# Optimization experiments

Hardware: AMD Instinct MI355X
Metric: run time of the kernel (lower is better)

## Reference

```python
import jax, jax.numpy as jnp
import numpy as np

B, N, DQ, DK, DV, H = 8, 1024, 512, 512, 512, 8
DH = DV // H  # 64


def setup_inputs() -> dict:
    key = jax.random.key(0)
    ks = jax.random.split(key, 12)
    Q = jax.random.normal(ks[0], (B, N, DQ), jnp.float32)
    K = jax.random.normal(ks[1], (B, N, DK), jnp.float32)
    U = jax.random.normal(ks[2], (H, N, N, B), jnp.float32) * 0.1  # additive bias, [H,Nq,Nk,B]
    mask = (jax.random.uniform(ks[3], (B, N)) < 0.9).astype(jnp.float32)
    w = 0.02
    return {
        'Q': Q, 'K': K, 'U': U, 'mask': mask,
        'Wq': jax.random.normal(ks[4], (DQ, DV), jnp.float32) * w,
        'bq': jnp.zeros((DV,), jnp.float32),
        'Wk': jax.random.normal(ks[5], (DK, DV), jnp.float32) * w,
        'bk': jnp.zeros((DV,), jnp.float32),
        'Wv': jax.random.normal(ks[6], (DK, DV), jnp.float32) * w,
        'bv': jnp.zeros((DV,), jnp.float32),
        'Wo': jax.random.normal(ks[7], (DV, DV), jnp.float32) * w,
        'bo': jnp.zeros((DV,), jnp.float32),
    }


def reference(Q, K, U, mask, Wq, bq, Wk, bk, Wv, bv, Wo, bo):
    m = mask[:, :, None]  # [B,N,1]
    q = (Q @ Wq + bq) * m  # [B,N,DV]
    k = (K @ Wk + bk) * m
    v = (K @ Wv + bv) * m
    # split heads: torch.cat(split(dh,2),0) is head-major -> [H,B,N,DH]
    qh = q.reshape(B, N, H, DH).transpose(2, 0, 1, 3)
    kh = k.reshape(B, N, H, DH).transpose(2, 0, 1, 3)
    vh = v.reshape(B, N, H, DH).transpose(2, 0, 1, 3)
    # U.transpose(1,3).transpose(-1,-2).reshape(H*B,N,N) == transpose(U,(0,3,1,2))
    bias = jnp.transpose(U, (0, 3, 1, 2))  # [H,B,Nq,Nk]
    scores = jnp.einsum('hbid,hbjd->hbij', qh, kh) / np.sqrt(DV) + bias
    # custom double-masked softmax (max taken over unmasked scores, faithfully)
    max_elem = jnp.max(scores, axis=3, keepdims=True)
    m1 = mask[None, :, :, None]  # [1,B,Nq,1]
    m2 = mask[None, :, None, :]  # [1,B,1,Nk]
    num = jnp.exp((scores - max_elem) * m1 * m2) * m1 * m2
    A = num / (jnp.sum(num, axis=3, keepdims=True) + 1e-16)
    o = qh + jnp.einsum('hbij,hbjd->hbid', A, vh)  # residual, [H,B,N,DH]
    O = o.transpose(1, 2, 0, 3).reshape(B, N, DV)  # merge heads
    O = O + jax.nn.relu((O @ Wo + bo) * m)
    return O
```

## Files before the change

### kernel.cpp

```cpp
#include <hip/hip_runtime.h>

#define B_   8
#define N_   1024
#define D_   512
#define H_   8
#define DH_  64
#define SCALE_ 0.044194173824159216f
#define LOG2E_ 1.4426950408889634f

typedef __attribute__((ext_vector_type(8))) short bf16x8;
typedef __attribute__((ext_vector_type(4))) float f32x4;
typedef __attribute__((ext_vector_type(8))) unsigned short us8;
typedef __attribute__((ext_vector_type(4))) unsigned int u32x4;

__device__ __forceinline__ unsigned short f2bf(float f) {
  unsigned u = __builtin_bit_cast(unsigned, f);
  u += 0x7fffu + ((u >> 16) & 1u);
  return (unsigned short)(u >> 16);
}
__device__ __forceinline__ float bf2f(unsigned short h) {
  unsigned u = ((unsigned)h) << 16;
  return __builtin_bit_cast(float, u);
}
__device__ __forceinline__ void gl_lds16(const void* g, void* l) {
  __builtin_amdgcn_global_load_lds(
      (const __attribute__((address_space(1))) unsigned int*)g,
      (__attribute__((address_space(3))) unsigned int*)l, 16, 0, 0);
}
__device__ __forceinline__ unsigned cvt_pk_bf16(float lo, float hi) {
  unsigned r;
  asm("v_cvt_pk_bf16_f32 %0, %1, %2" : "=v"(r) : "v"(lo), "v"(hi));
  return r;
}
#define MFMA16(a, b, c) __builtin_amdgcn_mfma_f32_16x16x32_bf16((a), (b), (c), 0, 0, 0)

__global__ void prep_w(const float* __restrict__ Wq, const float* __restrict__ Wk,
                       const float* __restrict__ Wv, const float* __restrict__ Wo,
                       unsigned short* __restrict__ WT) {
  int idx = blockIdx.x * 256 + threadIdx.x;
  int mat = idx >> 18;
  int rem = idx & 0x3FFFF;
  int k = rem >> 9, n = rem & 511;
  const float* W = (mat == 0) ? Wq : (mat == 1) ? Wk : (mat == 2) ? Wv : Wo;
  float v = W[(size_t)k * 512 + n];
  int kmap = (k & ~63) | ((k & 63) ^ ((n & 7) << 3));
  WT[(size_t)mat * 262144 + (size_t)n * 512 + kmap] = f2bf(v);
}

#define GEMM_BODY(A, W, bias, EPILOGUE)                                          \
  __shared__ unsigned short Alds[2][128][72];                                    \
  __shared__ unsigned short Blds[2][128 * 64];                                   \
  const int t = threadIdx.x, w = t >> 6, l = t & 63;                             \
  const int wr = w >> 1, wc = w & 1;                                             \
  const int lm = l & 15, lg = l >> 4;                                            \
  const int bm = blockIdx.x >> 2, bn = blockIdx.x & 3;                           \
  f32x4 acc[4][4];                                                               \
  _Pragma("unroll") for (int mt = 0; mt < 4; ++mt)                               \
  _Pragma("unroll") for (int nt = 0; nt < 4; ++nt)                               \
      acc[mt][nt] = f32x4{0.f, 0.f, 0.f, 0.f};                                   \
  float4 areg[8];                                                                \
  auto loadA = [&](int kt) {                                                     \
    _Pragma("unroll") for (int p = 0; p < 8; ++p) {                              \
      int row = (t >> 4) + p * 16, col = (t & 15) * 4;                           \
      areg[p] = *(const float4*)&A[((size_t)(bm * 128 + row)) * 512 + kt * 64 + col]; \
    }                                                                            \
  };                                                                             \
  auto issueB = [&](int kt, int sb) {                                            \
    _Pragma("unroll") for (int p = 0; p < 4; ++p) {                              \
      int chunk = w * 4 + p;                                                     \
      int row = chunk * 8 + (l >> 3), gc = kt * 64 + (l & 7) * 8;                \
      gl_lds16(&W[((size_t)(bn * 128 + row)) * 512 + gc],                        \
               &Blds[sb][chunk * 512 + l * 8]);                                  \
    }                                                                            \
  };                                                                             \
  auto writeA = [&](int sb) {                                                    \
    _Pragma("unroll") for (int p = 0; p < 8; ++p) {                              \
      int row = (t >> 4) + p * 16, col = (t & 15) * 4;                           \
      float4 v = areg[p];                                                        \
      uint2 d;                                                                   \
      d.x = (unsigned)f2bf(v.x) | ((unsigned)f2bf(v.y) << 16);                   \
      d.y = (unsigned)f2bf(v.z) | ((unsigned)f2bf(v.w) << 16);                   \
      *(uint2*)&Alds[sb][row][col] = d;                                          \
    }                                                                            \
  };                                                                             \
  loadA(0); issueB(0, 0); writeA(0);                                             \
  __syncthreads();                                                               \
  int buf = 0;                                                                   \
  for (int kt = 0; kt < 8; ++kt) {                                               \
    if (kt + 1 < 8) { loadA(kt + 1); issueB(kt + 1, buf ^ 1); }                  \
    _Pragma("unroll") for (int kk = 0; kk < 2; ++kk) {                           \
      bf16x8 af[4], bfv[4];                                                      \
      _Pragma("unroll") for (int mt = 0; mt < 4; ++mt)                           \
        af[mt] = *(const bf16x8*)&Alds[buf][wr * 64 + mt * 16 + lm][kk * 32 + lg * 8]; \
      _Pragma("unroll") for (int nt = 0; nt < 4; ++nt) {                         \
        int rr = wc * 64 + nt * 16 + lm;                                         \
        int c = (kk * 32 + lg * 8) ^ ((rr & 7) << 3);                            \
        bfv[nt] = *(const bf16x8*)&Blds[buf][rr * 64 + c];                       \
      }                                                                          \
      _Pragma("unroll") for (int mt = 0; mt < 4; ++mt)                           \
      _Pragma("unroll") for (int nt = 0; nt < 4; ++nt)                           \
          acc[mt][nt] = MFMA16(af[mt], bfv[nt], acc[mt][nt]);                    \
    }                                                                            \
    if (kt + 1 < 8) writeA(buf ^ 1);                                             \
    __syncthreads();                                                             \
    buf ^= 1;                                                                    \
  }                                                                              \
  _Pragma("unroll") for (int mt = 0; mt < 4; ++mt)                               \
  _Pragma("unroll") for (int nt = 0; nt < 4; ++nt) {                             \
    int gn = bn * 128 + wc * 64 + nt * 16 + lm;                                  \
    float bv_ = bias[gn];                                                        \
    _Pragma("unroll") for (int e = 0; e < 4; ++e) {                              \
      int gm = bm * 128 + wr * 64 + mt * 16 + lg * 4 + e;                        \
      float v = acc[mt][nt][e] + bv_;                                            \
      size_t off = (size_t)gm * 512 + gn;                                        \
      EPILOGUE                                                                   \
    }                                                                            \
  }

__global__ __launch_bounds__(256, 2) void gemm_proj3(
    const float* __restrict__ Q, const float* __restrict__ K,
    const unsigned short* __restrict__ WT,
    const float* __restrict__ bq, const float* __restrict__ bk,
    const float* __restrict__ bv, const float* __restrict__ mask,
    unsigned short* __restrict__ qb, unsigned short* __restrict__ kb,
    unsigned short* __restrict__ vtmp) {
  const int mat = blockIdx.y;
  const float* A = (mat == 0) ? Q : K;
  const unsigned short* W = WT + (size_t)mat * 262144;
  const float* bias = (mat == 0) ? bq : (mat == 1) ? bk : bv;
  unsigned short* outp = (mat == 0) ? qb : (mat == 1) ? kb : vtmp;
  GEMM_BODY(A, W, bias, { outp[off] = f2bf(v * mask[gm]); })
}

__global__ __launch_bounds__(256, 2) void gemm_final(
    const float* __restrict__ A, const unsigned short* __restrict__ W,
    const float* __restrict__ bias, const float* __restrict__ mask,
    const float* __restrict__ resid, float* __restrict__ outp) {
  GEMM_BODY(A, W, bias, { outp[off] = resid[off] + fmaxf(v, 0.f) * mask[gm]; })
}

__global__ void vtrans_kernel(const unsigned short* __restrict__ vtmp,
                              unsigned short* __restrict__ vT) {
  __shared__ unsigned short T[64][72];
  int b = blockIdx.x, ntile = blockIdx.y, dtile = blockIdx.z;
  int n0 = ntile * 64, d0 = dtile * 64;
  int t = threadIdx.x;
#pragma unroll
  for (int p = 0; p < 2; ++p) {
    int r = (t >> 3) + p * 32;
    int c = (t & 7) * 8;
    *(us8*)&T[r][c] = *(const us8*)&vtmp[((size_t)(b * N_ + n0 + r)) * D_ + d0 + c];
  }
  __syncthreads();
#pragma unroll
  for (int p = 0; p < 2; ++p) {
    int r = (t >> 3) + p * 32;
    int c = (t & 7) * 8;
    us8 v;
#pragma unroll
    for (int e = 0; e < 8; ++e) v[e] = T[c + e][r];
    *(us8*)&vT[((size_t)(b * D_ + d0 + r)) * N_ + n0 + c] = v;
  }
}

__global__ __launch_bounds__(512, 4) void attn_kernel(
    const unsigned short* __restrict__ qb, const unsigned short* __restrict__ kb,
    const unsigned short* __restrict__ vT, const float* __restrict__ U,
    const float* __restrict__ mask, float* __restrict__ O32) {
  __shared__ float Ulds[2][4096];
  __shared__ float Plds[8][16 * 36];
  const int t = threadIdx.x, w = t >> 6, l = t & 63;
  const int bid = (int)blockIdx.x;
  const int h = bid & 7;
  const int i0 = (bid >> 3) * 16;
  const int b = w;
  const int lm = l & 15, lg = l >> 4;

  const int sti = t >> 5, stj = t & 31;
  const float* Ug = U + (((size_t)h * N_ + i0 + sti) * N_ + stj) * B_;
  const int pbase = sti * 256 + ((stj ^ (sti >> 2)) & 31) * 8;
  const int bh0 = (stj >> 2) & 1;
  const int rot = stj & 3;

  float4 ua, ubv;
  auto stageLoad = [&](int jt) {
    const float* g = Ug + (size_t)jt * 256;
    ua  = *(const float4*)(g);
    ubv = *(const float4*)(g + 4);
  };
  auto rot4 = [&](float4 v) {
    if (rot & 1) v = float4{v.y, v.x, v.w, v.z};
    if (rot & 2) v = float4{v.z, v.w, v.x, v.y};
    return v;
  };
  auto stageWrite = [&](int sb) {
    *(float4*)&Ulds[sb][pbase + (0 ^ bh0) * 4] = rot4(ua);
    *(float4*)&Ulds[sb][pbase + (1 ^ bh0) * 4] = rot4(ubv);
  };

  const int ubase = ((lm ^ lg) * 8) + (((w >> 2) ^ ((lm >> 2) & 1)) * 4) + ((w & 3) ^ (lm & 3)) + lg * 1024;

  const unsigned short* Kb = kb + (size_t)b * N_ * D_ + h * DH_ + lg * 8;
  const unsigned short* Vb = vT + ((size_t)b * D_ + h * DH_ + lm) * N_ + lg * 8;
  const float* Mb = mask + b * N_ + lm;

  bf16x8 qf[2];
#pragma unroll
  for (int kt = 0; kt < 2; ++kt)
    qf[kt] = *(const bf16x8*)&qb[((size_t)b * N_ + i0 + lm) * D_ + h * DH_ + kt * 32 + lg * 8];

  f32x4 acc[4];
#pragma unroll
  for (int nt = 0; nt < 4; ++nt) acc[nt] = f32x4{0.f, 0.f, 0.f, 0.f};
  float lrun[4] = {0.f, 0.f, 0.f, 0.f};

  bf16x8 kf[2][2], vf[4];
  auto loadK = [&](int jt) {
#pragma unroll
    for (int j2 = 0; j2 < 2; ++j2)
#pragma unroll
      for (int kt = 0; kt < 2; ++kt)
        kf[j2][kt] = *(const bf16x8*)&Kb[(size_t)(jt * 32 + j2 * 16 + lm) * D_ + kt * 32];
  };

  stageLoad(0);
  stageWrite(0);
  loadK(0);
  __syncthreads();

  for (int jt = 0; jt < 32; ++jt) {
    const int buf = jt & 1;
    if (jt + 1 < 32) stageLoad(jt + 1);
#pragma unroll
    for (int nt = 0; nt < 4; ++nt)
      vf[nt] = *(const bf16x8*)&Vb[(size_t)nt * 16 * N_ + jt * 32];
    float mj0 = Mb[jt * 32];
    float mj1 = Mb[jt * 32 + 16];

    f32x4 S0 = f32x4{0.f, 0.f, 0.f, 0.f}, S1 = f32x4{0.f, 0.f, 0.f, 0.f};
#pragma unroll
    for (int kt = 0; kt < 2; ++kt) {
      S0 = MFMA16(qf[kt], kf[0][kt], S0);
      S1 = MFMA16(qf[kt], kf[1][kt], S1);
    }
    if (jt + 1 < 32) loadK(jt + 1);

#pragma unroll
    for (int e = 0; e < 4; ++e) {
      float u0 = Ulds[buf][e * 256 + ubase];
      float u1 = Ulds[buf][e * 256 + 128 + ubase];
      float s0 = S0[e] * SCALE_ + u0;
      float s1 = S1[e] * SCALE_ + u1;
      float p0 = (mj0 != 0.f) ? exp2f(s0 * LOG2E_) : 0.f;
      float p1 = (mj1 != 0.f) ? exp2f(s1 * LOG2E_) : 0.f;
      lrun[e] += p0 + p1;
      Plds[w][(lg * 4 + e) * 36 + lm] = p0;
      Plds[w][(lg * 4 + e) * 36 + lm + 16] = p1;
    }
    float4 pa0 = *(const float4*)&Plds[w][lm * 36 + lg * 8];
    float4 pa1 = *(const float4*)&Plds[w][lm * 36 + lg * 8 + 4];
    u32x4 pk;
    pk[0] = cvt_pk_bf16(pa0.x, pa0.y);
    pk[1] = cvt_pk_bf16(pa0.z, pa0.w);
    pk[2] = cvt_pk_bf16(pa1.x, pa1.y);
    pk[3] = cvt_pk_bf16(pa1.z, pa1.w);
    bf16x8 paf = __builtin_bit_cast(bf16x8, pk);
#pragma unroll
    for (int nt = 0; nt < 4; ++nt) acc[nt] = MFMA16(paf, vf[nt], acc[nt]);

    if (jt + 1 < 32) stageWrite(buf ^ 1);
    __syncthreads();
  }

#pragma unroll
  for (int e = 0; e < 4; ++e) {
    float lv = lrun[e];
    lv += __shfl_xor(lv, 1);
    lv += __shfl_xor(lv, 2);
    lv += __shfl_xor(lv, 4);
    lv += __shfl_xor(lv, 8);
    int gi = i0 + lg * 4 + e;
    float mi = mask[b * N_ + gi];
    float rD = 1.f / (lv + 1e-16f);
#pragma unroll
    for (int nt = 0; nt < 4; ++nt) {
      size_t off = ((size_t)b * N_ + gi) * D_ + h * DH_ + lm + nt * 16;
      float qv = bf2f(qb[off]);
      O32[off] = mi * (qv + acc[nt][e] * rD);
    }
  }
}

extern "C" void kernel_launch(void* const* d_in, const int* in_sizes, int n_in,
                              void* d_out, int out_size, void* d_ws, size_t ws_size,
                              hipStream_t stream) {
  const float* Q    = (const float*)d_in[0];
  const float* K    = (const float*)d_in[1];
  const float* U    = (const float*)d_in[2];
  const float* mask = (const float*)d_in[3];
  const float* Wq   = (const float*)d_in[4];
  const float* bq   = (const float*)d_in[5];
  const float* Wk   = (const float*)d_in[6];
  const float* bk   = (const float*)d_in[7];
  const float* Wv   = (const float*)d_in[8];
  const float* bv   = (const float*)d_in[9];
  const float* Wo   = (const float*)d_in[10];
  const float* bo   = (const float*)d_in[11];
  float* out = (float*)d_out;

  char* ws = (char*)d_ws;
  unsigned short* WT   = (unsigned short*)ws;
  unsigned short* qb   = (unsigned short*)(ws + (2llu << 20));
  unsigned short* kb   = (unsigned short*)(ws + (10llu << 20));
  unsigned short* vtmp = (unsigned short*)(ws + (18llu << 20));
  unsigned short* vTb  = (unsigned short*)(ws + (26llu << 20));
  float* O32           = (float*)(ws + (34llu << 20));

  prep_w<<<4096, 256, 0, stream>>>(Wq, Wk, Wv, Wo, WT);
  gemm_proj3<<<dim3(256, 3), 256, 0, stream>>>(Q, K, WT, bq, bk, bv, mask, qb, kb, vtmp);
  vtrans_kernel<<<dim3(8, 16, 8), 256, 0, stream>>>(vtmp, vTb);
  attn_kernel<<<512, 512, 0, stream>>>(qb, kb, vTb, U, mask, O32);
  gemm_final<<<256, 256, 0, stream>>>(O32, WT + 3 * 262144, bo, mask, O32, out);
}
```

Before: 240.4 us.

## Deepen U-bias prefetch to two tiles and pin attention loop schedule

New measurement: 232.1 us. 3.5% less time.

```diff
diff --git a/kernel.cpp b/kernel.cpp
--- a/kernel.cpp
+++ b/kernel.cpp
@@ -33,6 +33,7 @@
   return r;
 }
 #define MFMA16(a, b, c) __builtin_amdgcn_mfma_f32_16x16x32_bf16((a), (b), (c), 0, 0, 0)
+#define SCHED_PIN() __builtin_amdgcn_sched_barrier(0)
 
 __global__ void prep_w(const float* __restrict__ Wq, const float* __restrict__ Wk,
                        const float* __restrict__ Wv, const float* __restrict__ Wo,
@@ -167,7 +168,7 @@
     const unsigned short* __restrict__ qb, const unsigned short* __restrict__ kb,
     const unsigned short* __restrict__ vT, const float* __restrict__ U,
     const float* __restrict__ mask, float* __restrict__ O32) {
-  __shared__ float Ulds[2][4096];
+  __shared__ float Ulds[2 * 4096];
   __shared__ float Plds[8][16 * 36];
   const int t = threadIdx.x, w = t >> 6, l = t & 63;
   const int bid = (int)blockIdx.x;
@@ -182,20 +183,19 @@
   const int bh0 = (stj >> 2) & 1;
   const int rot = stj & 3;
 
-  float4 ua, ubv;
-  auto stageLoad = [&](int jt) {
-    const float* g = Ug + (size_t)jt * 256;
-    ua  = *(const float4*)(g);
-    ubv = *(const float4*)(g + 4);
-  };
   auto rot4 = [&](float4 v) {
     if (rot & 1) v = float4{v.y, v.x, v.w, v.z};
     if (rot & 2) v = float4{v.z, v.w, v.x, v.y};
     return v;
   };
-  auto stageWrite = [&](int sb) {
-    *(float4*)&Ulds[sb][pbase + (0 ^ bh0) * 4] = rot4(ua);
-    *(float4*)&Ulds[sb][pbase + (1 ^ bh0) * 4] = rot4(ubv);
+  auto stageLoad = [&](float4& a, float4& c, int jt) {
+    const float* g = Ug + (size_t)jt * 256;
+    a = *(const float4*)(g);
+    c = *(const float4*)(g + 4);
+  };
+  auto stageWrite = [&](const float4& a, const float4& c, int sb) {
+    *(float4*)&Ulds[sb * 4096 + pbase + (0 ^ bh0) * 4] = rot4(a);
+    *(float4*)&Ulds[sb * 4096 + pbase + (1 ^ bh0) * 4] = rot4(c);
   };
 
   const int ubase = ((lm ^ lg) * 8) + (((w >> 2) ^ ((lm >> 2) & 1)) * 4) + ((w & 3) ^ (lm & 3)) + lg * 1024;
@@ -223,54 +223,69 @@
         kf[j2][kt] = *(const bf16x8*)&Kb[(size_t)(jt * 32 + j2 * 16 + lm) * D_ + kt * 32];
   };
 
-  stageLoad(0);
-  stageWrite(0);
+  float4 uaA, ubA, uaB, ubB;
+  float mj0, mj1, mjn0, mjn1;
+
+  stageLoad(uaA, ubA, 0);
+  stageWrite(uaA, ubA, 0);
+  stageLoad(uaB, ubB, 1);
   loadK(0);
-  __syncthreads();
-
-  for (int jt = 0; jt < 32; ++jt) {
-    const int buf = jt & 1;
-    if (jt + 1 < 32) stageLoad(jt + 1);
-#pragma unroll
-    for (int nt = 0; nt < 4; ++nt)
-      vf[nt] = *(const bf16x8*)&Vb[(size_t)nt * 16 * N_ + jt * 32];
-    float mj0 = Mb[jt * 32];
-    float mj1 = Mb[jt * 32 + 16];
-
-    f32x4 S0 = f32x4{0.f, 0.f, 0.f, 0.f}, S1 = f32x4{0.f, 0.f, 0.f, 0.f};
-#pragma unroll
-    for (int kt = 0; kt < 2; ++kt) {
-      S0 = MFMA16(qf[kt], kf[0][kt], S0);
-      S1 = MFMA16(qf[kt], kf[1][kt], S1);
-    }
-    if (jt + 1 < 32) loadK(jt + 1);
-
-#pragma unroll
-    for (int e = 0; e < 4; ++e) {
-      float u0 = Ulds[buf][e * 256 + ubase];
-      float u1 = Ulds[buf][e * 256 + 128 + ubase];
-      float s0 = S0[e] * SCALE_ + u0;
-      float s1 = S1[e] * SCALE_ + u1;
-      float p0 = (mj0 != 0.f) ? exp2f(s0 * LOG2E_) : 0.f;
-      float p1 = (mj1 != 0.f) ? exp2f(s1 * LOG2E_) : 0.f;
-      lrun[e] += p0 + p1;
-      Plds[w][(lg * 4 + e) * 36 + lm] = p0;
-      Plds[w][(lg * 4 + e) * 36 + lm + 16] = p1;
-    }
-    float4 pa0 = *(const float4*)&Plds[w][lm * 36 + lg * 8];
-    float4 pa1 = *(const float4*)&Plds[w][lm * 36 + lg * 8 + 4];
-    u32x4 pk;
-    pk[0] = cvt_pk_bf16(pa0.x, pa0.y);
-    pk[1] = cvt_pk_bf16(pa0.z, pa0.w);
-    pk[2] = cvt_pk_bf16(pa1.x, pa1.y);
-    pk[3] = cvt_pk_bf16(pa1.z, pa1.w);
-    bf16x8 paf = __builtin_bit_cast(bf16x8, pk);
-#pragma unroll
-    for (int nt = 0; nt < 4; ++nt) acc[nt] = MFMA16(paf, vf[nt], acc[nt]);
-
-    if (jt + 1 < 32) stageWrite(buf ^ 1);
-    __syncthreads();
-  }
+  mj0 = Mb[0]; mj1 = Mb[16];
+  SCHED_PIN();
+  asm volatile("s_waitcnt lgkmcnt(0)");
+  __builtin_amdgcn_sched_barrier(0);
+  __builtin_amdgcn_s_barrier();
+
+#define ATTN_BODY(T, BUFR, SWa, SWb, SLa, SLb)                                   \
+  {                                                                              \
+    _Pragma("unroll") for (int nt = 0; nt < 4; ++nt)                             \
+      vf[nt] = *(const bf16x8*)&Vb[(size_t)nt * 16 * N_ + (T) * 32];             \
+    SCHED_PIN();                                                                 \
+    f32x4 S0 = f32x4{0.f, 0.f, 0.f, 0.f}, S1 = f32x4{0.f, 0.f, 0.f, 0.f};       \
+    _Pragma("unroll") for (int kt = 0; kt < 2; ++kt) {                           \
+      S0 = MFMA16(qf[kt], kf[0][kt], S0);                                        \
+      S1 = MFMA16(qf[kt], kf[1][kt], S1);                                        \
+    }                                                                            \
+    if ((T) + 1 < 32) {                                                          \
+      loadK((T) + 1);                                                            \
+      mjn0 = Mb[((T) + 1) * 32]; mjn1 = Mb[((T) + 1) * 32 + 16];                 \
+    }                                                                            \
+    SCHED_PIN();                                                                 \
+    _Pragma("unroll") for (int e = 0; e < 4; ++e) {                              \
+      float u0 = Ulds[(BUFR) * 4096 + e * 256 + ubase];                          \
+      float u1 = Ulds[(BUFR) * 4096 + e * 256 + 128 + ubase];                    \
+      float s0 = S0[e] * SCALE_ + u0;                                            \
+      float s1 = S1[e] * SCALE_ + u1;                                            \
+      float p0 = (mj0 != 0.f) ? exp2f(s0 * LOG2E_) : 0.f;                        \
+      float p1 = (mj1 != 0.f) ? exp2f(s1 * LOG2E_) : 0.f;                        \
+      lrun[e] += p0 + p1;                                                        \
+      Plds[w][(lg * 4 + e) * 36 + lm] = p0;                                      \
+      Plds[w][(lg * 4 + e) * 36 + lm + 16] = p1;                                 \
+    }                                                                            \
+    float4 pa0 = *(const float4*)&Plds[w][lm * 36 + lg * 8];                     \
+    float4 pa1 = *(const float4*)&Plds[w][lm * 36 + lg * 8 + 4];                 \
+    u32x4 pk;                                                                    \
+    pk[0] = cvt_pk_bf16(pa0.x, pa0.y);                                           \
+    pk[1] = cvt_pk_bf16(pa0.z, pa0.w);                                           \
+    pk[2] = cvt_pk_bf16(pa1.x, pa1.y);                                           \
+    pk[3] = cvt_pk_bf16(pa1.z, pa1.w);                                           \
+    bf16x8 paf = __builtin_bit_cast(bf16x8, pk);                                 \
+    _Pragma("unroll") for (int nt = 0; nt < 4; ++nt)                             \
+      acc[nt] = MFMA16(paf, vf[nt], acc[nt]);                                    \
+    if ((T) + 1 < 32) stageWrite(SWa, SWb, (BUFR) ^ 1);                          \
+    if ((T) + 2 < 32) stageLoad(SLa, SLb, (T) + 2);                              \
+    mj0 = mjn0; mj1 = mjn1;                                                      \
+    SCHED_PIN();                                                                 \
+    asm volatile("s_waitcnt lgkmcnt(0)");                                        \
+    __builtin_amdgcn_sched_barrier(0);                                           \
+    __builtin_amdgcn_s_barrier();                                                \
+  }
+
+  for (int jt = 0; jt < 32; jt += 2) {
+    ATTN_BODY(jt,     0, uaB, ubB, uaA, ubA)
+    ATTN_BODY(jt + 1, 1, uaA, ubA, uaB, ubB)
+  }
+#undef ATTN_BODY
 
 #pragma unroll
   for (int e = 0; e < 4; ++e) {
```
